# Optimization experiments

Hardware: AMD Instinct MI355X
Metric: run time of the kernel (lower is better)

The kernel has to match this reference:

```python
import jax, jax.numpy as jnp
import numpy as np

N, SEQ, E, R = 2048, 128, 512, 128


def setup_inputs() -> dict:
    key = jax.random.key(0)
    ks = jax.random.split(key, 8)
    C = jnp.sort(jax.random.randint(ks[0], (N, 2), 0, SEQ), axis=-1)  # start <= end
    L = jax.random.normal(ks[1], (N, SEQ, E), dtype=jnp.float32)
    Pos_weights = jnp.ones((N, SEQ), dtype=jnp.float32)
    Neg_weights = jnp.ones((N, SEQ), dtype=jnp.float32)
    s1 = 1.0 / np.sqrt(E)
    s2 = 1.0 / np.sqrt(R)
    W1p = jax.random.normal(ks[2], (E, R), dtype=jnp.float32) * s1
    W2p = jax.random.normal(ks[3], (R, R), dtype=jnp.float32) * s2
    W1n = jax.random.normal(ks[4], (E, R), dtype=jnp.float32) * s1
    W2n = jax.random.normal(ks[5], (R, R), dtype=jnp.float32) * s2
    Wa = jax.random.normal(ks[6], (E, R), dtype=jnp.float32) * s1
    z = jnp.zeros((R,), dtype=jnp.float32)
    return {
        'C': C, 'L': L, 'Pos_weights': Pos_weights, 'Neg_weights': Neg_weights,
        'W1p': W1p, 'b1p': z, 'W2p': W2p, 'b2p': z,
        'W1n': W1n, 'b1n': z, 'W2n': W2n, 'b2n': z,
        'Wa': Wa, 'ba': z,
    }


def _safe_cdist(x, y):
    # Euclidean distance matrix with torch.cdist semantics; zero subgradient at d=0.
    d2 = (jnp.sum(x * x, -1)[:, None] + jnp.sum(y * y, -1)[None, :]
          - 2.0 * x @ y.T)
    d2 = jnp.maximum(d2, 0.0)
    safe = jnp.where(d2 > 0, d2, 1.0)
    return jnp.where(d2 > 0, jnp.sqrt(safe), 0.0)


def _mlp2(x, W1, b1, W2, b2):
    return jnp.tanh(jnp.tanh(x @ W1 + b1) @ W2 + b2)


def reference(C, L, Pos_weights, Neg_weights,
              W1p, b1p, W2p, b2p, W1n, b1n, W2n, b2n, Wa, ba):
    t = jnp.arange(SEQ)[None, :]                  # [1, SEQ]
    start = C[:, 0:1]
    end = C[:, 1:2]
    in_region = (t >= start) & (t <= end)         # [N, SEQ]
    pos_mask = jnp.where(in_region, Pos_weights, 0.0)
    neg_mask = jnp.where(in_region, 0.0, Neg_weights)
    Pos_rep = pos_mask[..., None] * L             # [N, SEQ, E]
    Neg_rep = neg_mask[..., None] * L
    pos_t = _mlp2(Pos_rep, W1p, b1p, W2p, b2p).mean(axis=1)  # [N, R]
    neg_t = _mlp2(Neg_rep, W1n, b1n, W2n, b2n).mean(axis=1)  # [N, R]
    pos_sim = jnp.exp(-_safe_cdist(pos_t, pos_t)).sum()
    neg_sim = jnp.exp(-_safe_cdist(pos_t, neg_t)).sum()
    loss = -jnp.log(pos_sim / neg_sim)
    final_feature = jnp.tanh((Pos_rep + Neg_rep) @ Wa + ba).mean(axis=1)  # [N, R]
    return final_feature, loss
```

## Files before the change

### kernel.cpp

```cpp
#include <hip/hip_runtime.h>
#include <math.h>

#define N_   2048
#define SEQ_ 128
#define E_   512
#define R_   128
#define NR_  (N_ * R_)

typedef __attribute__((ext_vector_type(8))) short short8;
typedef __attribute__((ext_vector_type(4))) float f32x4;

typedef __attribute__((address_space(3))) void lds_t;
typedef __attribute__((address_space(1))) const void glb_t;

__device__ __forceinline__ void async16(void* l, const void* g) {
    __builtin_amdgcn_global_load_lds((glb_t*)g, (lds_t*)l, 16, 0, 0);
}

__device__ __forceinline__ ushort f2bf(float f) {
    union { float f; uint u; } v; v.f = f;
    uint r = v.u + 0x7FFFu + ((v.u >> 16) & 1u);
    return (ushort)(r >> 16);
}
__device__ __forceinline__ float fast_tanhf(float x) {
    float ax = fabsf(x);
    float t = __expf(-2.f * ax);
    float r = (1.f - t) / (1.f + t);
    return copysignf(r, x);
}

__global__ void prep_kernel(const float* __restrict__ W1p, const float* __restrict__ W1n,
                            const float* __restrict__ Wa,  const float* __restrict__ W2p,
                            const float* __restrict__ W2n, ushort* __restrict__ WT)
{
    int idx = blockIdx.x * 256 + threadIdx.x;
    if (idx < 196608) {
        int m = idx >> 16;
        int o = idx & 65535;
        int r = o >> 9, e = o & 511;
        const float* src = (m == 0) ? W1p : (m == 1) ? W1n : Wa;
        WT[idx] = f2bf(src[e * R_ + r]);
    } else if (idx < 229376) {
        int o = idx - 196608;
        int m = o >> 14;
        int p = o & 16383;
        int r = p >> 7, e = p & 127;
        const float* src = (m == 0) ? W2p : W2n;
        WT[idx] = f2bf(src[e * R_ + r]);
    }
}

__global__ __launch_bounds__(256, 2)
void mlp_mfma_kernel(const int* __restrict__ C, const float* __restrict__ L,
                     const float* __restrict__ Pw, const float* __restrict__ Nw,
                     const float* __restrict__ b1p, const float* __restrict__ b2p,
                     const float* __restrict__ b1n, const float* __restrict__ b2n,
                     const float* __restrict__ ba,  const ushort* __restrict__ WT,
                     float* __restrict__ pp, float* __restrict__ nn,
                     float* __restrict__ aa)
{
    __shared__ __align__(16) ushort lds[28672];
    __shared__ float sPm[64], sNm[64];

    ushort* sX  = lds;
    ushort* sW  = lds + 4096;
    ushort* sH1 = lds;
    ushort* sW2 = lds + 8192;

    const ushort* W2pT = WT + 196608;
    const ushort* W2nT = WT + 212992;

    const int bid = blockIdx.x;
    const int n = bid >> 1, half = bid & 1;
    const int tid = threadIdx.x;
    const int w = tid >> 6, l = tid & 63, q = l >> 4, c = l & 15;

    if (tid < 64) {
        int tg = half * 64 + tid;
        int c0 = C[2 * n], c1 = C[2 * n + 1];
        bool in = (tg >= c0) && (tg <= c1);
        sPm[tid] = in ? Pw[n * SEQ_ + tg] : 0.f;
        sNm[tid] = in ? 0.f : Nw[n * SEQ_ + tg];
    }

    f32x4 accP[4][2], accN[4][2], accA[4][2];
#pragma unroll
    for (int mt = 0; mt < 4; ++mt)
#pragma unroll
        for (int nt = 0; nt < 2; ++nt) { accP[mt][nt] = 0.f; accN[mt][nt] = 0.f; accA[mt][nt] = 0.f; }

    const float* Lbase = L + ((size_t)n * SEQ_ + half * 64) * E_;

    for (int ch = 0; ch < 8; ++ch) {
        const int kb = ch * 64;
#pragma unroll
        for (int it = 0; it < 2; ++it) {
            int sidx = it * 256 + tid;
            int row = sidx >> 3, seg = sidx & 7;
            const float* gp = Lbase + row * E_ + kb + seg * 8;
            float4 v0 = *(const float4*)gp;
            float4 v1 = *(const float4*)(gp + 4);
            union { short8 v; ushort u[8]; } t8;
            t8.u[0] = f2bf(v0.x); t8.u[1] = f2bf(v0.y); t8.u[2] = f2bf(v0.z); t8.u[3] = f2bf(v0.w);
            t8.u[4] = f2bf(v1.x); t8.u[5] = f2bf(v1.y); t8.u[6] = f2bf(v1.z); t8.u[7] = f2bf(v1.w);
            *(short8*)&sX[row * 64 + (seg ^ (row & 7)) * 8] = t8.v;
        }
#pragma unroll
        for (int j = 0; j < 12; ++j) {
            int gi = j * 4 + w;
            int s = gi >> 4, blk = gi & 15;
            int row = blk * 8 + (l >> 3);
            int kseg = (l & 7) ^ (row & 7);
            async16(&sW[(s * 128 + blk * 8) * 64], WT + s * 65536 + row * E_ + kb + kseg * 8);
        }
        __syncthreads();

#pragma unroll
        for (int k2 = 0; k2 < 2; ++k2) {
            short8 a[4];
#pragma unroll
            for (int mt = 0; mt < 4; ++mt) {
                int row = mt * 16 + c;
                a[mt] = *(const short8*)&sX[row * 64 + ((k2 * 4 + q) ^ (row & 7)) * 8];
            }
#pragma unroll
            for (int nt = 0; nt < 2; ++nt) {
                int r = w * 32 + nt * 16 + c;
                int p = (k2 * 4 + q) ^ (r & 7);
                short8 bP = *(const short8*)&sW[(0 * 128 + r) * 64 + p * 8];
                short8 bN = *(const short8*)&sW[(1 * 128 + r) * 64 + p * 8];
                short8 bA = *(const short8*)&sW[(2 * 128 + r) * 64 + p * 8];
#pragma unroll
                for (int mt = 0; mt < 4; ++mt) {
                    accP[mt][nt] = __builtin_amdgcn_mfma_f32_16x16x32_bf16(a[mt], bP, accP[mt][nt], 0, 0, 0);
                    accN[mt][nt] = __builtin_amdgcn_mfma_f32_16x16x32_bf16(a[mt], bN, accN[mt][nt], 0, 0, 0);
                    accA[mt][nt] = __builtin_amdgcn_mfma_f32_16x16x32_bf16(a[mt], bA, accA[mt][nt], 0, 0, 0);
                }
            }
        }
        __syncthreads();
    }

#pragma unroll
    for (int nt = 0; nt < 2; ++nt) {
        int r = w * 32 + nt * 16 + c;
        float bar = ba[r];
        float s = 0.f;
#pragma unroll
        for (int mt = 0; mt < 4; ++mt)
#pragma unroll
            for (int i = 0; i < 4; ++i) {
                int t = mt * 16 + q * 4 + i;
                float m = sPm[t] + sNm[t];
                s += fast_tanhf(fmaf(m, accA[mt][nt][i], bar));
            }
        s += __shfl_xor(s, 16);
        s += __shfl_xor(s, 32);
        if (q == 0) aa[half * NR_ + n * R_ + r] = s * (1.f / SEQ_);
    }

    for (int ps = 0; ps < 2; ++ps) {
        const f32x4 (*acc1)[2] = ps ? accN : accP;
        const float* sM  = ps ? sNm : sPm;
        const float* b1  = ps ? b1n : b1p;
        const float* b2  = ps ? b2n : b2p;
        const ushort* W2T = ps ? W2nT : W2pT;
        float* outp = ps ? nn : pp;

        __syncthreads();
#pragma unroll
        for (int nt = 0; nt < 2; ++nt) {
            int r = w * 32 + nt * 16 + c;
            float b1r = b1[r];
            int seg = r >> 3;
#pragma unroll
            for (int mt = 0; mt < 4; ++mt)
#pragma unroll
                for (int i = 0; i < 4; ++i) {
                    int t = mt * 16 + q * 4 + i;
                    float h = fast_tanhf(fmaf(sM[t], acc1[mt][nt][i], b1r));
                    sH1[t * 128 + (seg ^ (t & 7)) * 8 + (r & 7)] = f2bf(h);
                }
        }
#pragma unroll
        for (int j = 0; j < 8; ++j) {
            int gi = j * 4 + w;
            int row = gi * 4 + (l >> 4);
            int kseg = (l & 15) ^ (row & 7);
            async16(&sW2[gi * 512], W2T + row * 128 + kseg * 8);
        }
        __syncthreads();

        f32x4 acc2[4][2];
#pragma unroll
        for (int mt = 0; mt < 4; ++mt)
#pragma unroll
            for (int nt = 0; nt < 2; ++nt) acc2[mt][nt] = 0.f;

#pragma unroll
        for (int k2 = 0; k2 < 4; ++k2) {
            short8 af[4];
#pragma unroll
            for (int mt = 0; mt < 4; ++mt) {
                int row = mt * 16 + c;
                af[mt] = *(const short8*)&sH1[row * 128 + ((k2 * 4 + q) ^ (row & 7)) * 8];
            }
#pragma unroll
            for (int nt = 0; nt < 2; ++nt) {
                int r = w * 32 + nt * 16 + c;
                short8 bf_ = *(const short8*)&sW2[r * 128 + ((k2 * 4 + q) ^ (r & 7)) * 8];
#pragma unroll
                for (int mt = 0; mt < 4; ++mt)
                    acc2[mt][nt] = __builtin_amdgcn_mfma_f32_16x16x32_bf16(af[mt], bf_, acc2[mt][nt], 0, 0, 0);
            }
        }
#pragma unroll
        for (int nt = 0; nt < 2; ++nt) {
            int r = w * 32 + nt * 16 + c;
            float b2r = b2[r];
            float s = 0.f;
#pragma unroll
            for (int mt = 0; mt < 4; ++mt)
#pragma unroll
                for (int i = 0; i < 4; ++i)
                    s += fast_tanhf(acc2[mt][nt][i] + b2r);
            s += __shfl_xor(s, 16);
            s += __shfl_xor(s, 32);
            if (q == 0) outp[half * NR_ + n * R_ + r] = s * (1.f / SEQ_);
        }
    }
}

__global__ __launch_bounds__(256)
void ffcomb_kernel(const float* __restrict__ aa, float* __restrict__ out)
{
    int i = (blockIdx.x * 256 + threadIdx.x) * 4;
    float4 a0 = *(const float4*)(aa + i);
    float4 a1 = *(const float4*)(aa + NR_ + i);
    float4 o; o.x = a0.x + a1.x; o.y = a0.y + a1.y; o.z = a0.z + a1.z; o.w = a0.w + a1.w;
    *(float4*)(out + i) = o;
}

__global__ __launch_bounds__(256, 2)
void sim_kernel(const float* __restrict__ pp, const float* __restrict__ nn,
                float* __restrict__ simP, float* __restrict__ simN)
{
    __shared__ __align__(16) float sPi[64][133];
    __shared__ __align__(16) float sPj[32][133];
    __shared__ __align__(16) float sNj[32][133];

    const int jb = blockIdx.x;
    const int ib = blockIdx.y;
    const int tid = threadIdx.x;

#pragma unroll
    for (int it = 0; it < 8; ++it) {
        int idx = it * 256 + tid;
        int row = idx >> 5, seg = idx & 31;
        int g = (ib * 64 + row) * R_ + seg * 4;
        float4 a = *(const float4*)(pp + g);
        float4 b = *(const float4*)(pp + NR_ + g);
        a.x += b.x; a.y += b.y; a.z += b.z; a.w += b.w;
        *(float4*)&sPi[row][seg * 4] = a;
    }
#pragma unroll
    for (int it = 0; it < 4; ++it) {
        int idx = it * 256 + tid;
        int row = idx >> 5, seg = idx & 31;
        int g = (jb * 32 + row) * R_ + seg * 4;
        float4 a = *(const float4*)(pp + g);
        float4 b = *(const float4*)(pp + NR_ + g);
        a.x += b.x; a.y += b.y; a.z += b.z; a.w += b.w;
        *(float4*)&sPj[row][seg * 4] = a;
        float4 u = *(const float4*)(nn + g);
        float4 v = *(const float4*)(nn + NR_ + g);
        u.x += v.x; u.y += v.y; u.z += v.z; u.w += v.w;
        *(float4*)&sNj[row][seg * 4] = u;
    }
    __syncthreads();

    const int ty = tid >> 4, tx = tid & 15;
    float d2p[4][2] = {}, d2n[4][2] = {};

    for (int rr = 0; rr < R_; rr += 4) {
        float4 xi[4], pj[2], nj[2];
#pragma unroll
        for (int a = 0; a < 4; ++a) xi[a] = *(const float4*)&sPi[ty * 4 + a][rr];
#pragma unroll
        for (int b = 0; b < 2; ++b) {
            pj[b] = *(const float4*)&sPj[tx * 2 + b][rr];
            nj[b] = *(const float4*)&sNj[tx * 2 + b][rr];
        }
#pragma unroll
        for (int a = 0; a < 4; ++a)
#pragma unroll
            for (int b = 0; b < 2; ++b) {
                float dx;
                dx = xi[a].x - pj[b].x; d2p[a][b] = fmaf(dx, dx, d2p[a][b]);
                dx = xi[a].y - pj[b].y; d2p[a][b] = fmaf(dx, dx, d2p[a][b]);
                dx = xi[a].z - pj[b].z; d2p[a][b] = fmaf(dx, dx, d2p[a][b]);
                dx = xi[a].w - pj[b].w; d2p[a][b] = fmaf(dx, dx, d2p[a][b]);
                dx = xi[a].x - nj[b].x; d2n[a][b] = fmaf(dx, dx, d2n[a][b]);
                dx = xi[a].y - nj[b].y; d2n[a][b] = fmaf(dx, dx, d2n[a][b]);
                dx = xi[a].z - nj[b].z; d2n[a][b] = fmaf(dx, dx, d2n[a][b]);
                dx = xi[a].w - nj[b].w; d2n[a][b] = fmaf(dx, dx, d2n[a][b]);
            }
    }

    float sp = 0.f, sn = 0.f;
#pragma unroll
    for (int a = 0; a < 4; ++a)
#pragma unroll
        for (int b = 0; b < 2; ++b) {
            sp += __expf(-sqrtf(d2p[a][b]));
            sn += __expf(-sqrtf(d2n[a][b]));
        }

#pragma unroll
    for (int off = 32; off; off >>= 1) {
        sp += __shfl_down(sp, off);
        sn += __shfl_down(sn, off);
    }
    __shared__ float redP[4], redN[4];
    const int wave = tid >> 6, lane = tid & 63;
    if (lane == 0) { redP[wave] = sp; redN[wave] = sn; }
    __syncthreads();
    if (tid == 0) {
        int bidl = ib * 64 + jb;
        simP[bidl] = redP[0] + redP[1] + redP[2] + redP[3];
        simN[bidl] = redN[0] + redN[1] + redN[2] + redN[3];
    }
}

__global__ __launch_bounds__(256)
void finalize_kernel(const float* __restrict__ simP, const float* __restrict__ simN,
                     float* __restrict__ out)
{
    const int tid = threadIdx.x;
    double sp = 0.0, sn = 0.0;
    for (int i = tid; i < 2048; i += 256) { sp += (double)simP[i]; sn += (double)simN[i]; }
    __shared__ double rp[256], rn[256];
    rp[tid] = sp; rn[tid] = sn;
    __syncthreads();
    for (int s = 128; s; s >>= 1) {
        if (tid < s) { rp[tid] += rp[tid + s]; rn[tid] += rn[tid + s]; }
        __syncthreads();
    }
    if (tid == 0) out[NR_] = (float)(-log(rp[0] / rn[0]));
}

extern "C" void kernel_launch(void* const* d_in, const int* in_sizes, int n_in,
                              void* d_out, int out_size, void* d_ws, size_t ws_size,
                              hipStream_t stream)
{
    const int*   C   = (const int*)  d_in[0];
    const float* L   = (const float*)d_in[1];
    const float* Pw  = (const float*)d_in[2];
    const float* Nw  = (const float*)d_in[3];
    const float* W1p = (const float*)d_in[4];
    const float* b1p = (const float*)d_in[5];
    const float* W2p = (const float*)d_in[6];
    const float* b2p = (const float*)d_in[7];
    const float* W1n = (const float*)d_in[8];
    const float* b1n = (const float*)d_in[9];
    const float* W2n = (const float*)d_in[10];
    const float* b2n = (const float*)d_in[11];
    const float* Wa  = (const float*)d_in[12];
    const float* ba  = (const float*)d_in[13];

    float* out = (float*)d_out;
    float* pp  = (float*)d_ws;
    float* nn  = pp + 2 * NR_;
    float* aa  = nn + 2 * NR_;
    float* simP = aa + 2 * NR_;
    float* simN = simP + 2048;
    ushort* WT = (ushort*)((char*)d_ws + 6 * (size_t)NR_ * 4 + 65536);

    hipLaunchKernelGGL(prep_kernel, dim3(896), dim3(256), 0, stream,
                       W1p, W1n, Wa, W2p, W2n, WT);
    hipLaunchKernelGGL(mlp_mfma_kernel, dim3(2 * N_), dim3(256), 0, stream,
                       C, L, Pw, Nw, b1p, b2p, b1n, b2n, ba, WT, pp, nn, aa);
    hipLaunchKernelGGL(ffcomb_kernel, dim3(NR_ / 1024), dim3(256), 0, stream, aa, out);
    hipLaunchKernelGGL(sim_kernel, dim3(64, 32), dim3(256), 0, stream,
                       pp, nn, simP, simN);
    hipLaunchKernelGGL(finalize_kernel, dim3(1), dim3(256), 0, stream, simP, simN, out);
}
```

Baseline: 888.6 us.

## Skip masked-out MFMA tiles and software-pipeline L chunk loads

```diff
diff --git a/kernel.cpp b/kernel.cpp
--- a/kernel.cpp
+++ b/kernel.cpp
@@ -31,8 +31,21 @@
 
 __global__ void prep_kernel(const float* __restrict__ W1p, const float* __restrict__ W1n,
                             const float* __restrict__ Wa,  const float* __restrict__ W2p,
-                            const float* __restrict__ W2n, ushort* __restrict__ WT)
-{
+                            const float* __restrict__ W2n, const float* __restrict__ b1p,
+                            const float* __restrict__ b1n, ushort* __restrict__ WT,
+                            float* __restrict__ c2)
+{
+    if (blockIdx.x == 896) {
+        int t = threadIdx.x;
+        int ps = t >> 7, r = t & 127;
+        const float* W2 = ps ? W2n : W2p;
+        const float* b1 = ps ? b1n : b1p;
+        float s = 0.f;
+        for (int k = 0; k < 128; ++k)
+            s += tanhf(b1[k]) * W2[k * R_ + r];
+        c2[ps * R_ + r] = s;
+        return;
+    }
     int idx = blockIdx.x * 256 + threadIdx.x;
     if (idx < 196608) {
         int m = idx >> 16;
@@ -56,6 +69,7 @@
                      const float* __restrict__ b1p, const float* __restrict__ b2p,
                      const float* __restrict__ b1n, const float* __restrict__ b2n,
                      const float* __restrict__ ba,  const ushort* __restrict__ WT,
+                     const float* __restrict__ c2,
                      float* __restrict__ pp, float* __restrict__ nn,
                      float* __restrict__ aa)
 {
@@ -75,14 +89,25 @@
     const int tid = threadIdx.x;
     const int w = tid >> 6, l = tid & 63, q = l >> 4, c = l & 15;
 
+    const int c0 = C[2 * n], c1 = C[2 * n + 1];
+
     if (tid < 64) {
         int tg = half * 64 + tid;
-        int c0 = C[2 * n], c1 = C[2 * n + 1];
         bool in = (tg >= c0) && (tg <= c1);
         sPm[tid] = in ? Pw[n * SEQ_ + tg] : 0.f;
         sNm[tid] = in ? 0.f : Nw[n * SEQ_ + tg];
     }
 
+    bool needP[4], needN[4];
+    bool anyP = false, anyN = false;
+#pragma unroll
+    for (int mt = 0; mt < 4; ++mt) {
+        int lo = half * 64 + mt * 16, hi = lo + 15;
+        needP[mt] = (hi >= c0) && (lo <= c1);
+        needN[mt] = !((lo >= c0) && (hi <= c1));
+        anyP |= needP[mt]; anyN |= needN[mt];
+    }
+
     f32x4 accP[4][2], accN[4][2], accA[4][2];
 #pragma unroll
     for (int mt = 0; mt < 4; ++mt)
@@ -90,30 +115,53 @@
         for (int nt = 0; nt < 2; ++nt) { accP[mt][nt] = 0.f; accN[mt][nt] = 0.f; accA[mt][nt] = 0.f; }
 
     const float* Lbase = L + ((size_t)n * SEQ_ + half * 64) * E_;
+
+    const int xrow = tid >> 3, xseg = tid & 7;
+    const int xst0 = xrow * 64 + (xseg ^ (xrow & 7)) * 8;
+    const int xst1 = xst0 + 32 * 64;
+    const float* gpA = Lbase + xrow * E_ + xseg * 8;
+
+    float4 xv0, xv1, xv2, xv3;
+    {
+        const float* g0 = gpA;
+        const float* g1 = gpA + 32 * E_;
+        xv0 = *(const float4*)g0; xv1 = *(const float4*)(g0 + 4);
+        xv2 = *(const float4*)g1; xv3 = *(const float4*)(g1 + 4);
+    }
 
     for (int ch = 0; ch < 8; ++ch) {
         const int kb = ch * 64;
-#pragma unroll
-        for (int it = 0; it < 2; ++it) {
-            int sidx = it * 256 + tid;
-            int row = sidx >> 3, seg = sidx & 7;
-            const float* gp = Lbase + row * E_ + kb + seg * 8;
-            float4 v0 = *(const float4*)gp;
-            float4 v1 = *(const float4*)(gp + 4);
-            union { short8 v; ushort u[8]; } t8;
-            t8.u[0] = f2bf(v0.x); t8.u[1] = f2bf(v0.y); t8.u[2] = f2bf(v0.z); t8.u[3] = f2bf(v0.w);
-            t8.u[4] = f2bf(v1.x); t8.u[5] = f2bf(v1.y); t8.u[6] = f2bf(v1.z); t8.u[7] = f2bf(v1.w);
-            *(short8*)&sX[row * 64 + (seg ^ (row & 7)) * 8] = t8.v;
-        }
 #pragma unroll
         for (int j = 0; j < 12; ++j) {
             int gi = j * 4 + w;
             int s = gi >> 4, blk = gi & 15;
+            if (s == 0 && !anyP) continue;
+            if (s == 1 && !anyN) continue;
             int row = blk * 8 + (l >> 3);
             int kseg = (l & 7) ^ (row & 7);
             async16(&sW[(s * 128 + blk * 8) * 64], WT + s * 65536 + row * E_ + kb + kseg * 8);
         }
-        __syncthreads();
+        {
+            union { short8 v; ushort u[8]; } t8;
+            t8.u[0] = f2bf(xv0.x); t8.u[1] = f2bf(xv0.y); t8.u[2] = f2bf(xv0.z); t8.u[3] = f2bf(xv0.w);
+            t8.u[4] = f2bf(xv1.x); t8.u[5] = f2bf(xv1.y); t8.u[6] = f2bf(xv1.z); t8.u[7] = f2bf(xv1.w);
+            *(short8*)&sX[xst0] = t8.v;
+            t8.u[0] = f2bf(xv2.x); t8.u[1] = f2bf(xv2.y); t8.u[2] = f2bf(xv2.z); t8.u[3] = f2bf(xv2.w);
+            t8.u[4] = f2bf(xv3.x); t8.u[5] = f2bf(xv3.y); t8.u[6] = f2bf(xv3.z); t8.u[7] = f2bf(xv3.w);
+            *(short8*)&sX[xst1] = t8.v;
+        }
+        __builtin_amdgcn_sched_barrier(0);
+        if (ch < 7) {
+            const float* g0 = gpA + kb + 64;
+            const float* g1 = g0 + 32 * E_;
+            xv0 = *(const float4*)g0; xv1 = *(const float4*)(g0 + 4);
+            xv2 = *(const float4*)g1; xv3 = *(const float4*)(g1 + 4);
+            asm volatile("s_waitcnt vmcnt(4) lgkmcnt(0)" ::: "memory");
+        } else {
+            asm volatile("s_waitcnt vmcnt(0) lgkmcnt(0)" ::: "memory");
+        }
+        __builtin_amdgcn_s_barrier();
+        __builtin_amdgcn_sched_barrier(0);
 
 #pragma unroll
         for (int k2 = 0; k2 < 2; ++k2) {
@@ -123,22 +171,41 @@
                 int row = mt * 16 + c;
                 a[mt] = *(const short8*)&sX[row * 64 + ((k2 * 4 + q) ^ (row & 7)) * 8];
             }
-#pragma unroll
-            for (int nt = 0; nt < 2; ++nt) {
-                int r = w * 32 + nt * 16 + c;
-                int p = (k2 * 4 + q) ^ (r & 7);
-                short8 bP = *(const short8*)&sW[(0 * 128 + r) * 64 + p * 8];
-                short8 bN = *(const short8*)&sW[(1 * 128 + r) * 64 + p * 8];
-                short8 bA = *(const short8*)&sW[(2 * 128 + r) * 64 + p * 8];
-#pragma unroll
-                for (int mt = 0; mt < 4; ++mt) {
-                    accP[mt][nt] = __builtin_amdgcn_mfma_f32_16x16x32_bf16(a[mt], bP, accP[mt][nt], 0, 0, 0);
-                    accN[mt][nt] = __builtin_amdgcn_mfma_f32_16x16x32_bf16(a[mt], bN, accN[mt][nt], 0, 0, 0);
-                    accA[mt][nt] = __builtin_amdgcn_mfma_f32_16x16x32_bf16(a[mt], bA, accA[mt][nt], 0, 0, 0);
-                }
-            }
-        }
-        __syncthreads();
+            const int r0 = w * 32 + c;
+            const int r1 = r0 + 16;
+            const int p0 = (k2 * 4 + q) ^ (r0 & 7);
+            short8 bA0 = *(const short8*)&sW[(256 + r0) * 64 + p0 * 8];
+            short8 bA1 = *(const short8*)&sW[(256 + r1) * 64 + p0 * 8];
+#pragma unroll
+            for (int mt = 0; mt < 4; ++mt) {
+                accA[mt][0] = __builtin_amdgcn_mfma_f32_16x16x32_bf16(a[mt], bA0, accA[mt][0], 0, 0, 0);
+                accA[mt][1] = __builtin_amdgcn_mfma_f32_16x16x32_bf16(a[mt], bA1, accA[mt][1], 0, 0, 0);
+            }
+            if (anyP) {
+                short8 bP0 = *(const short8*)&sW[r0 * 64 + p0 * 8];
+                short8 bP1 = *(const short8*)&sW[r1 * 64 + p0 * 8];
+#pragma unroll
+                for (int mt = 0; mt < 4; ++mt)
+                    if (needP[mt]) {
+                        accP[mt][0] = __builtin_amdgcn_mfma_f32_16x16x32_bf16(a[mt], bP0, accP[mt][0], 0, 0, 0);
+                        accP[mt][1] = __builtin_amdgcn_mfma_f32_16x16x32_bf16(a[mt], bP1, accP[mt][1], 0, 0, 0);
+                    }
+            }
+            if (anyN) {
+                short8 bN0 = *(const short8*)&sW[(128 + r0) * 64 + p0 * 8];
+                short8 bN1 = *(const short8*)&sW[(128 + r1) * 64 + p0 * 8];
+#pragma unroll
+                for (int mt = 0; mt < 4; ++mt)
+                    if (needN[mt]) {
+                        accN[mt][0] = __builtin_amdgcn_mfma_f32_16x16x32_bf16(a[mt], bN0, accN[mt][0], 0, 0, 0);
+                        accN[mt][1] = __builtin_amdgcn_mfma_f32_16x16x32_bf16(a[mt], bN1, accN[mt][1], 0, 0, 0);
+                    }
+            }
+        }
+        if (ch < 7) asm volatile("s_waitcnt vmcnt(4) lgkmcnt(0)" ::: "memory");
+        else        asm volatile("s_waitcnt vmcnt(0) lgkmcnt(0)" ::: "memory");
+        __builtin_amdgcn_s_barrier();
+        __builtin_amdgcn_sched_barrier(0);
     }
 
 #pragma unroll
@@ -159,37 +226,18 @@
         if (q == 0) aa[half * NR_ + n * R_ + r] = s * (1.f / SEQ_);
     }
 
+#pragma unroll
     for (int ps = 0; ps < 2; ++ps) {
         const f32x4 (*acc1)[2] = ps ? accN : accP;
         const float* sM  = ps ? sNm : sPm;
         const float* b1  = ps ? b1n : b1p;
         const float* b2  = ps ? b2n : b2p;
         const ushort* W2T = ps ? W2nT : W2pT;
+        const float* c2x = c2 + ps * R_;
         float* outp = ps ? nn : pp;
-
-        __syncthreads();
-#pragma unroll
-        for (int nt = 0; nt < 2; ++nt) {
-            int r = w * 32 + nt * 16 + c;
-            float b1r = b1[r];
-            int seg = r >> 3;
-#pragma unroll
-            for (int mt = 0; mt < 4; ++mt)
-#pragma unroll
-                for (int i = 0; i < 4; ++i) {
-                    int t = mt * 16 + q * 4 + i;
-                    float h = fast_tanhf(fmaf(sM[t], acc1[mt][nt][i], b1r));
-                    sH1[t * 128 + (seg ^ (t & 7)) * 8 + (r & 7)] = f2bf(h);
-                }
-        }
-#pragma unroll
-        for (int j = 0; j < 8; ++j) {
-            int gi = j * 4 + w;
-            int row = gi * 4 + (l >> 4);
-            int kseg = (l & 15) ^ (row & 7);
-            async16(&sW2[gi * 512], W2T + row * 128 + kseg * 8);
-        }
-        __syncthreads();
+        const bool any = ps ? anyN : anyP;
+        const bool nd[4] = { ps ? needN[0] : needP[0], ps ? needN[1] : needP[1],
+                             ps ? needN[2] : needP[2], ps ? needN[3] : needP[3] };
 
         f32x4 acc2[4][2];
 #pragma unroll
@@ -197,33 +245,66 @@
 #pragma unroll
             for (int nt = 0; nt < 2; ++nt) acc2[mt][nt] = 0.f;
 
-#pragma unroll
-        for (int k2 = 0; k2 < 4; ++k2) {
-            short8 af[4];
-#pragma unroll
-            for (int mt = 0; mt < 4; ++mt) {
-                int row = mt * 16 + c;
-                af[mt] = *(const short8*)&sH1[row * 128 + ((k2 * 4 + q) ^ (row & 7)) * 8];
-            }
+        if (any) {
+            __syncthreads();
 #pragma unroll
             for (int nt = 0; nt < 2; ++nt) {
                 int r = w * 32 + nt * 16 + c;
-                short8 bf_ = *(const short8*)&sW2[r * 128 + ((k2 * 4 + q) ^ (r & 7)) * 8];
-#pragma unroll
-                for (int mt = 0; mt < 4; ++mt)
-                    acc2[mt][nt] = __builtin_amdgcn_mfma_f32_16x16x32_bf16(af[mt], bf_, acc2[mt][nt], 0, 0, 0);
-            }
-        }
+                float b1r = b1[r];
+                int seg = r >> 3;
+#pragma unroll
+                for (int mt = 0; mt < 4; ++mt) {
+                    if (!nd[mt]) continue;
+#pragma unroll
+                    for (int i = 0; i < 4; ++i) {
+                        int t = mt * 16 + q * 4 + i;
+                        float m = sM[t];
+                        float h = (m == 0.f) ? 0.f : fast_tanhf(fmaf(m, acc1[mt][nt][i], b1r));
+                        sH1[t * 128 + (seg ^ (t & 7)) * 8 + (r & 7)] = f2bf(h);
+                    }
+                }
+            }
+#pragma unroll
+            for (int j = 0; j < 8; ++j) {
+                int gi = j * 4 + w;
+                int row = gi * 4 + (l >> 4);
+                int kseg = (l & 15) ^ (row & 7);
+                async16(&sW2[gi * 512], W2T + row * 128 + kseg * 8);
+            }
+            __syncthreads();
+
+#pragma unroll
+            for (int k2 = 0; k2 < 4; ++k2) {
+                const int r0 = w * 32 + c;
+                const int r1 = r0 + 16;
+                const int p0 = (k2 * 4 + q) ^ (r0 & 7);
+                short8 bf0 = *(const short8*)&sW2[r0 * 128 + p0 * 8];
+                short8 bf1 = *(const short8*)&sW2[r1 * 128 + p0 * 8];
+#pragma unroll
+                for (int mt = 0; mt < 4; ++mt) {
+                    if (!nd[mt]) continue;
+                    int row = mt * 16 + c;
+                    short8 af = *(const short8*)&sH1[row * 128 + ((k2 * 4 + q) ^ (row & 7)) * 8];
+                    acc2[mt][0] = __builtin_amdgcn_mfma_f32_16x16x32_bf16(af, bf0, acc2[mt][0], 0, 0, 0);
+                    acc2[mt][1] = __builtin_amdgcn_mfma_f32_16x16x32_bf16(af, bf1, acc2[mt][1], 0, 0, 0);
+                }
+            }
+        }
+
 #pragma unroll
         for (int nt = 0; nt < 2; ++nt) {
             int r = w * 32 + nt * 16 + c;
             float b2r = b2[r];
+            float tc = fast_tanhf(c2x[r] + b2r);
             float s = 0.f;
 #pragma unroll
             for (int mt = 0; mt < 4; ++mt)
 #pragma unroll
-                for (int i = 0; i < 4; ++i)
-                    s += fast_tanhf(acc2[mt][nt][i] + b2r);
+                for (int i = 0; i < 4; ++i) {
+                    int t = mt * 16 + q * 4 + i;
+                    float m = sM[t];
+                    s += (m == 0.f) ? tc : fast_tanhf(acc2[mt][nt][i] + b2r);
+                }
             s += __shfl_xor(s, 16);
             s += __shfl_xor(s, 32);
             if (q == 0) outp[half * NR_ + n * R_ + r] = s * (1.f / SEQ_);
@@ -375,11 +456,12 @@
     float* simP = aa + 2 * NR_;
     float* simN = simP + 2048;
     ushort* WT = (ushort*)((char*)d_ws + 6 * (size_t)NR_ * 4 + 65536);
-
-    hipLaunchKernelGGL(prep_kernel, dim3(896), dim3(256), 0, stream,
-                       W1p, W1n, Wa, W2p, W2n, WT);
+    float* c2  = (float*)(WT + 229376);
+
+    hipLaunchKernelGGL(prep_kernel, dim3(897), dim3(256), 0, stream,
+                       W1p, W1n, Wa, W2p, W2n, b1p, b1n, WT, c2);
     hipLaunchKernelGGL(mlp_mfma_kernel, dim3(2 * N_), dim3(256), 0, stream,
-                       C, L, Pw, Nw, b1p, b2p, b1n, b2n, ba, WT, pp, nn, aa);
+                       C, L, Pw, Nw, b1p, b2p, b1n, b2n, ba, WT, c2, pp, nn, aa);
     hipLaunchKernelGGL(ffcomb_kernel, dim3(NR_ / 1024), dim3(256), 0, stream, aa, out);
     hipLaunchKernelGGL(sim_kernel, dim3(64, 32), dim3(256), 0, stream,
                        pp, nn, simP, simN);
```

Measured after the change: 930.2 us. +4.7%, slower.

## Repartition MLP MFMA tiles by rows per wave, loading activations directly to registers

Applied to the files above, without the earlier changes.

```diff
diff --git a/kernel.cpp b/kernel.cpp
--- a/kernel.cpp
+++ b/kernel.cpp
@@ -50,7 +50,7 @@
     }
 }
 
-__global__ __launch_bounds__(256, 2)
+__global__ __launch_bounds__(256, 3)
 void mlp_mfma_kernel(const int* __restrict__ C, const float* __restrict__ L,
                      const float* __restrict__ Pw, const float* __restrict__ Nw,
                      const float* __restrict__ b1p, const float* __restrict__ b2p,
@@ -59,13 +59,9 @@
                      float* __restrict__ pp, float* __restrict__ nn,
                      float* __restrict__ aa)
 {
-    __shared__ __align__(16) ushort lds[28672];
+    __shared__ __align__(16) ushort lds[24576];
+    __shared__ float sRed[4][128];
     __shared__ float sPm[64], sNm[64];
-
-    ushort* sX  = lds;
-    ushort* sW  = lds + 4096;
-    ushort* sH1 = lds;
-    ushort* sW2 = lds + 8192;
 
     const ushort* W2pT = WT + 196608;
     const ushort* W2nT = WT + 212992;
@@ -83,150 +79,147 @@
         sNm[tid] = in ? 0.f : Nw[n * SEQ_ + tg];
     }
 
-    f32x4 accP[4][2], accN[4][2], accA[4][2];
-#pragma unroll
-    for (int mt = 0; mt < 4; ++mt)
-#pragma unroll
-        for (int nt = 0; nt < 2; ++nt) { accP[mt][nt] = 0.f; accN[mt][nt] = 0.f; accA[mt][nt] = 0.f; }
-
-    const float* Lbase = L + ((size_t)n * SEQ_ + half * 64) * E_;
+    f32x4 accP[8], accN[8], accA[8];
+#pragma unroll
+    for (int nt = 0; nt < 8; ++nt) { accP[nt] = 0.f; accN[nt] = 0.f; accA[nt] = 0.f; }
+
+    const float* Lrow = L + ((size_t)(n * SEQ_ + half * 64 + w * 16 + c)) * E_ + q * 8;
 
     for (int ch = 0; ch < 8; ++ch) {
         const int kb = ch * 64;
-#pragma unroll
-        for (int it = 0; it < 2; ++it) {
-            int sidx = it * 256 + tid;
-            int row = sidx >> 3, seg = sidx & 7;
-            const float* gp = Lbase + row * E_ + kb + seg * 8;
-            float4 v0 = *(const float4*)gp;
-            float4 v1 = *(const float4*)(gp + 4);
-            union { short8 v; ushort u[8]; } t8;
-            t8.u[0] = f2bf(v0.x); t8.u[1] = f2bf(v0.y); t8.u[2] = f2bf(v0.z); t8.u[3] = f2bf(v0.w);
-            t8.u[4] = f2bf(v1.x); t8.u[5] = f2bf(v1.y); t8.u[6] = f2bf(v1.z); t8.u[7] = f2bf(v1.w);
-            *(short8*)&sX[row * 64 + (seg ^ (row & 7)) * 8] = t8.v;
-        }
 #pragma unroll
         for (int j = 0; j < 12; ++j) {
             int gi = j * 4 + w;
             int s = gi >> 4, blk = gi & 15;
             int row = blk * 8 + (l >> 3);
             int kseg = (l & 7) ^ (row & 7);
-            async16(&sW[(s * 128 + blk * 8) * 64], WT + s * 65536 + row * E_ + kb + kseg * 8);
+            async16(&lds[(s * 128 + blk * 8) * 64], WT + s * 65536 + row * E_ + kb + kseg * 8);
+        }
+        const float* p0 = Lrow + kb;
+        float4 xa = *(const float4*)p0;
+        float4 xb = *(const float4*)(p0 + 4);
+        float4 xc = *(const float4*)(p0 + 32);
+        float4 xd = *(const float4*)(p0 + 36);
+        short8 af0, af1;
+        {
+            union { short8 v; ushort u[8]; } t8;
+            t8.u[0] = f2bf(xa.x); t8.u[1] = f2bf(xa.y); t8.u[2] = f2bf(xa.z); t8.u[3] = f2bf(xa.w);
+            t8.u[4] = f2bf(xb.x); t8.u[5] = f2bf(xb.y); t8.u[6] = f2bf(xb.z); t8.u[7] = f2bf(xb.w);
+            af0 = t8.v;
+            t8.u[0] = f2bf(xc.x); t8.u[1] = f2bf(xc.y); t8.u[2] = f2bf(xc.z); t8.u[3] = f2bf(xc.w);
+            t8.u[4] = f2bf(xd.x); t8.u[5] = f2bf(xd.y); t8.u[6] = f2bf(xd.z); t8.u[7] = f2bf(xd.w);
+            af1 = t8.v;
         }
         __syncthreads();
 
 #pragma unroll
         for (int k2 = 0; k2 < 2; ++k2) {
-            short8 a[4];
-#pragma unroll
-            for (int mt = 0; mt < 4; ++mt) {
-                int row = mt * 16 + c;
-                a[mt] = *(const short8*)&sX[row * 64 + ((k2 * 4 + q) ^ (row & 7)) * 8];
-            }
-#pragma unroll
-            for (int nt = 0; nt < 2; ++nt) {
-                int r = w * 32 + nt * 16 + c;
-                int p = (k2 * 4 + q) ^ (r & 7);
-                short8 bP = *(const short8*)&sW[(0 * 128 + r) * 64 + p * 8];
-                short8 bN = *(const short8*)&sW[(1 * 128 + r) * 64 + p * 8];
-                short8 bA = *(const short8*)&sW[(2 * 128 + r) * 64 + p * 8];
-#pragma unroll
-                for (int mt = 0; mt < 4; ++mt) {
-                    accP[mt][nt] = __builtin_amdgcn_mfma_f32_16x16x32_bf16(a[mt], bP, accP[mt][nt], 0, 0, 0);
-                    accN[mt][nt] = __builtin_amdgcn_mfma_f32_16x16x32_bf16(a[mt], bN, accN[mt][nt], 0, 0, 0);
-                    accA[mt][nt] = __builtin_amdgcn_mfma_f32_16x16x32_bf16(a[mt], bA, accA[mt][nt], 0, 0, 0);
-                }
+            short8 a = k2 ? af1 : af0;
+            const int p = ((k2 * 4 + q) ^ (c & 7)) * 8;
+#pragma unroll
+            for (int nt = 0; nt < 8; ++nt) {
+                int ro = (nt * 16 + c) * 64 + p;
+                short8 bP = *(const short8*)&lds[ro];
+                short8 bN = *(const short8*)&lds[8192 + ro];
+                short8 bA = *(const short8*)&lds[16384 + ro];
+                accP[nt] = __builtin_amdgcn_mfma_f32_16x16x32_bf16(a, bP, accP[nt], 0, 0, 0);
+                accN[nt] = __builtin_amdgcn_mfma_f32_16x16x32_bf16(a, bN, accN[nt], 0, 0, 0);
+                accA[nt] = __builtin_amdgcn_mfma_f32_16x16x32_bf16(a, bA, accA[nt], 0, 0, 0);
             }
         }
         __syncthreads();
     }
 
 #pragma unroll
-    for (int nt = 0; nt < 2; ++nt) {
-        int r = w * 32 + nt * 16 + c;
+    for (int nt = 0; nt < 8; ++nt) {
+        int r = nt * 16 + c;
         float bar = ba[r];
         float s = 0.f;
 #pragma unroll
-        for (int mt = 0; mt < 4; ++mt)
-#pragma unroll
-            for (int i = 0; i < 4; ++i) {
-                int t = mt * 16 + q * 4 + i;
-                float m = sPm[t] + sNm[t];
-                s += fast_tanhf(fmaf(m, accA[mt][nt][i], bar));
-            }
+        for (int i = 0; i < 4; ++i) {
+            int t = w * 16 + q * 4 + i;
+            float m = sPm[t] + sNm[t];
+            s += fast_tanhf(fmaf(m, accA[nt][i], bar));
+        }
         s += __shfl_xor(s, 16);
         s += __shfl_xor(s, 32);
-        if (q == 0) aa[half * NR_ + n * R_ + r] = s * (1.f / SEQ_);
-    }
-
-    for (int ps = 0; ps < 2; ++ps) {
-        const f32x4 (*acc1)[2] = ps ? accN : accP;
-        const float* sM  = ps ? sNm : sPm;
-        const float* b1  = ps ? b1n : b1p;
-        const float* b2  = ps ? b2n : b2p;
-        const ushort* W2T = ps ? W2nT : W2pT;
-        float* outp = ps ? nn : pp;
-
-        __syncthreads();
-#pragma unroll
-        for (int nt = 0; nt < 2; ++nt) {
-            int r = w * 32 + nt * 16 + c;
-            float b1r = b1[r];
-            int seg = r >> 3;
-#pragma unroll
-            for (int mt = 0; mt < 4; ++mt)
+        if (q == 0) sRed[w][r] = s;
+    }
+    __syncthreads();
+    if (tid < 128) {
+        float v = sRed[0][tid] + sRed[1][tid] + sRed[2][tid] + sRed[3][tid];
+        aa[half * NR_ + n * R_ + tid] = v * (1.f / SEQ_);
+    }
+
+    {
+        ushort* sH1w = &lds[16384 + w * 2048];
+
+#pragma unroll
+        for (int ps = 0; ps < 2; ++ps) {
+            const float* sM  = ps ? sNm : sPm;
+            const float* b1  = ps ? b1n : b1p;
+            const float* b2  = ps ? b2n : b2p;
+            const ushort* W2T = ps ? W2nT : W2pT;
+            float* outp = ps ? nn : pp;
+
+            __syncthreads();
+
+#pragma unroll
+            for (int nt = 0; nt < 8; ++nt) {
+                int r = nt * 16 + c;
+                float b1r = b1[r];
+                int rseg = r >> 3;
 #pragma unroll
                 for (int i = 0; i < 4; ++i) {
-                    int t = mt * 16 + q * 4 + i;
-                    float h = fast_tanhf(fmaf(sM[t], acc1[mt][nt][i], b1r));
-                    sH1[t * 128 + (seg ^ (t & 7)) * 8 + (r & 7)] = f2bf(h);
+                    int t = q * 4 + i;
+                    float m = sM[w * 16 + t];
+                    float acc = ps ? accN[nt][i] : accP[nt][i];
+                    float h = fast_tanhf(fmaf(m, acc, b1r));
+                    int seg = rseg ^ (t & 7);
+                    sH1w[t * 128 + seg * 8 + (c & 7)] = f2bf(h);
                 }
-        }
-#pragma unroll
-        for (int j = 0; j < 8; ++j) {
-            int gi = j * 4 + w;
-            int row = gi * 4 + (l >> 4);
-            int kseg = (l & 15) ^ (row & 7);
-            async16(&sW2[gi * 512], W2T + row * 128 + kseg * 8);
-        }
-        __syncthreads();
-
-        f32x4 acc2[4][2];
-#pragma unroll
-        for (int mt = 0; mt < 4; ++mt)
-#pragma unroll
-            for (int nt = 0; nt < 2; ++nt) acc2[mt][nt] = 0.f;
-
-#pragma unroll
-        for (int k2 = 0; k2 < 4; ++k2) {
-            short8 af[4];
-#pragma unroll
-            for (int mt = 0; mt < 4; ++mt) {
-                int row = mt * 16 + c;
-                af[mt] = *(const short8*)&sH1[row * 128 + ((k2 * 4 + q) ^ (row & 7)) * 8];
-            }
-#pragma unroll
-            for (int nt = 0; nt < 2; ++nt) {
-                int r = w * 32 + nt * 16 + c;
-                short8 bf_ = *(const short8*)&sW2[r * 128 + ((k2 * 4 + q) ^ (r & 7)) * 8];
-#pragma unroll
-                for (int mt = 0; mt < 4; ++mt)
-                    acc2[mt][nt] = __builtin_amdgcn_mfma_f32_16x16x32_bf16(af[mt], bf_, acc2[mt][nt], 0, 0, 0);
-            }
-        }
-#pragma unroll
-        for (int nt = 0; nt < 2; ++nt) {
-            int r = w * 32 + nt * 16 + c;
-            float b2r = b2[r];
-            float s = 0.f;
-#pragma unroll
-            for (int mt = 0; mt < 4; ++mt)
+            }
+#pragma unroll
+            for (int j = 0; j < 8; ++j) {
+                int gi = j * 4 + w;
+                int row = gi * 4 + (l >> 4);
+                int kseg = (l & 15) ^ (row & 7);
+                async16(&lds[gi * 512], W2T + row * 128 + kseg * 8);
+            }
+            __syncthreads();
+
+            f32x4 acc2[8];
+#pragma unroll
+            for (int nt = 0; nt < 8; ++nt) acc2[nt] = 0.f;
+
+#pragma unroll
+            for (int k2 = 0; k2 < 4; ++k2) {
+                const int p = ((k2 * 4 + q) ^ (c & 7)) * 8;
+                short8 a = *(const short8*)&sH1w[c * 128 + p];
+#pragma unroll
+                for (int nt = 0; nt < 8; ++nt) {
+                    short8 b = *(const short8*)&lds[(nt * 16 + c) * 128 + p];
+                    acc2[nt] = __builtin_amdgcn_mfma_f32_16x16x32_bf16(a, b, acc2[nt], 0, 0, 0);
+                }
+            }
+
+#pragma unroll
+            for (int nt = 0; nt < 8; ++nt) {
+                int r = nt * 16 + c;
+                float b2r = b2[r];
+                float s = 0.f;
 #pragma unroll
                 for (int i = 0; i < 4; ++i)
-                    s += fast_tanhf(acc2[mt][nt][i] + b2r);
-            s += __shfl_xor(s, 16);
-            s += __shfl_xor(s, 32);
-            if (q == 0) outp[half * NR_ + n * R_ + r] = s * (1.f / SEQ_);
+                    s += fast_tanhf(acc2[nt][i] + b2r);
+                s += __shfl_xor(s, 16);
+                s += __shfl_xor(s, 32);
+                if (q == 0) sRed[w][r] = s;
+            }
+            __syncthreads();
+            if (tid < 128) {
+                float v = sRed[0][tid] + sRed[1][tid] + sRed[2][tid] + sRed[3][tid];
+                outp[half * NR_ + n * R_ + tid] = v * (1.f / SEQ_);
+            }
         }
     }
 }
```

Result: slower. 920.7 us (+3.6%).
